# Kernel optimization log

Hardware: AMD Instinct MI355X
Metric: run time of the kernel (lower is better)

## Reference

```python
import jax, jax.numpy as jnp
import numpy as np
from jax import lax

KSIZE = 3      # match kernel
STRIDE = 1
RATE = 2       # dilation / downscale rate
FUSE_K = 3     # diagonal-fuse kernel
SCALE = 10.0   # softmax scale
FUSE = True
ESC = 1e-4     # escape_NaN, added per-element before the reduce_sum (as in torch code)


def _same_pad(x, k, s):
    # x: [C, H, W] -> zero-padded so that strided k-window 'same' extraction works
    C, H, W = x.shape
    oh, ow = -(-H // s), -(-W // s)
    ph = max(0, (oh - 1) * s + k - H)
    pw = max(0, (ow - 1) * s + k - W)
    xp = jnp.pad(x, ((0, 0), (ph // 2, ph - ph // 2), (pw // 2, pw - pw // 2)))
    return xp, oh, ow


def extract_patches(x, k, s):
    # x: [C, H, W] -> [L, C, k, k], L row-major over output grid (matches torch Unfold)
    C = x.shape[0]
    xp, oh, ow = _same_pad(x, k, s)
    cols = [xp[:, dh:dh + s * (oh - 1) + 1:s, dw:dw + s * (ow - 1) + 1:s]
            for dh in range(k) for dw in range(k)]
    p = jnp.stack(cols, 0).reshape(k, k, C, oh, ow)
    return p.transpose(3, 4, 2, 0, 1).reshape(oh * ow, C, k, k)


def fuse_diag(x):
    # conv with eye(FUSE_K) kernel, 'same' padding: sum of diagonal shifts
    A, B = x.shape
    pt = (FUSE_K - 1) // 2
    pb = FUSE_K - 1 - pt
    xp = jnp.pad(x, ((pt, pb), (pt, pb)))
    out = xp[0:A, 0:B]
    for d in range(1, FUSE_K):
        out = out + xp[d:d + A, d:d + B]
    return out


def _forward(f, b, mask):
    B, C, H, W = f.shape
    kernel = 2 * RATE
    # mask -> mm gate over background patches (shared across batch: torch uses m[0])
    mask_s = mask[0][:, ::4 * RATE, ::4 * RATE]           # [1, H/r, W/r] nearest downsample
    m = extract_patches(mask_s, KSIZE, STRIDE)            # [L, 1, k, k]
    mm = (jnp.mean(m, axis=(1, 2, 3)) == 0.0).astype(f.dtype)[:, None, None]  # [L,1,1]

    def single(fi, bi):
        # raw patches from full-res background for reconstruction: [Lb, C, 2r, 2r]
        raw_w = extract_patches(bi, kernel, RATE * STRIDE)
        # nearest 1/rate downsample
        fs = fi[:, ::RATE, ::RATE]
        bs = bi[:, ::RATE, ::RATE]
        bh, bw = bs.shape[1], bs.shape[2]
        fh, fw = fs.shape[1], fs.shape[2]
        Lb, Lf = bh * bw, fh * fw
        # match patches from downsampled background, L2-normalized per patch
        w = extract_patches(bs, KSIZE, STRIDE)                      # [Lb, C, 3, 3]
        denom = jnp.sqrt(jnp.sum(w * w + ESC, axis=(1, 2, 3), keepdims=True))
        wn = (w / denom).reshape(Lb, -1)                            # [Lb, C*9]
        # correlation = conv of fs with wn filters = patch GEMM
        fp = extract_patches(fs, KSIZE, 1).reshape(Lf, -1)          # [Lf, C*9]
        scores = wn @ fp.T                                          # [Lb, Lf]
        if FUSE:
            s = fuse_diag(scores)
            s = s.reshape(bh, bw, fh, fw).transpose(1, 0, 3, 2).reshape(Lb, Lf)
            s = fuse_diag(s)
            s = s.reshape(bw, bh, fw, fh).transpose(1, 0, 3, 2).reshape(Lb, Lf)
            scores = s
        att = scores.reshape(Lb, fh, fw) * mm
        att = jax.nn.softmax(att * SCALE, axis=0) * mm              # softmax over patches
        # conv_transpose2d(att, raw_w, stride=rate, padding=1) / 4
        rhs = jnp.flip(raw_w, (2, 3)).transpose(1, 0, 2, 3)         # [C, Lb, 2r, 2r] OIHW
        pad = kernel - 1 - 1                                        # k - 1 - torch_padding
        out = lax.conv_general_dilated(
            att[None], rhs, window_strides=(1, 1),
            padding=[(pad, pad), (pad, pad)], lhs_dilation=(RATE, RATE),
            dimension_numbers=('NCHW', 'OIHW', 'NCHW'))[0] / 4.0    # [C, H, W]
        return out

    return jax.vmap(single)(f, b)


def setup_inputs() -> dict:
    key = jax.random.key(0)
    k1, k2 = jax.random.split(key)
    B, C, H, W = 4, 128, 96, 96
    f = jax.random.normal(k1, (B, C, H, W), jnp.float32)
    b = jax.random.normal(k2, (B, C, H, W), jnp.float32)
    mask = jnp.zeros((1, 1, 4 * H, 4 * W), jnp.float32)
    mask = mask.at[:, :, 96:288, 96:288].set(1.0)
    return {"f": f, "b": b, "mask": mask}


def reference(f, b, mask):
    return _forward(f, b, mask)
```

## Files before the change

### kernel.cpp

```cpp
#include <hip/hip_runtime.h>

typedef _Float16 half8 __attribute__((ext_vector_type(8)));
typedef float floatx4 __attribute__((ext_vector_type(4)));

#define LBF 2304
#define K1  1152
#define LDK2 2304

__device__ __forceinline__ void gll16(const _Float16* g, _Float16* l) {
    __builtin_amdgcn_global_load_lds((const __attribute__((address_space(1))) void*)g,
                                     (__attribute__((address_space(3))) void*)l, 16, 0, 0);
}

__device__ __forceinline__ int dec_kc(int s) { return (s >= 0) ? s + 1 : -s - 1; }

__global__ void stage_scan(const float* __restrict__ f, const float* __restrict__ bsrc,
                           const float* __restrict__ mask,
                           float* __restrict__ ds, int* __restrict__ pos) {
    int tid = threadIdx.x;
    if (blockIdx.x < 9216) {
        long flat = (long)blockIdx.x * 256 + tid;
        int p = flat % 2304;
        long rest = flat / 2304;
        int c = rest % 128;
        int b = (rest / 128) % 4;
        int t = rest / (128 * 4);
        int pi = p / 48, pj = p % 48;
        const float* src = t ? bsrc : f;
        ds[flat] = src[(((long)b * 128 + c) * 96 + 2 * pi) * 96 + 2 * pj];
        return;
    }
    int mmb[9], loc[9]; int s = 0;
#pragma unroll
    for (int t = 0; t < 9; t++) {
        int p = tid * 9 + t;
        int pi = p / 48, pj = p % 48;
        float sm = 0.f;
#pragma unroll
        for (int u = 0; u < 3; u++)
#pragma unroll
            for (int v = 0; v < 3; v++) {
                int y = pi - 1 + u, x = pj - 1 + v;
                if ((unsigned)y < 48u && (unsigned)x < 48u)
                    sm += mask[(8 * y) * 384 + 8 * x];
            }
        int m = (sm == 0.f) ? 1 : 0;
        mmb[t] = m; loc[t] = s; s += m;
    }
    __shared__ int sh[256];
    sh[tid] = s; __syncthreads();
    for (int off = 1; off < 256; off <<= 1) {
        int v = (tid >= off) ? sh[tid - off] : 0;
        __syncthreads();
        sh[tid] += v;
        __syncthreads();
    }
    int excl = sh[tid] - s;
#pragma unroll
    for (int t = 0; t < 9; t++) {
        int e = excl + loc[t];
        pos[tid * 9 + t] = mmb[t] ? e : (-e - 1);
    }
}

__global__ void prep_fp(const float* __restrict__ ds, _Float16* __restrict__ fp) {
    int k = blockIdx.x * 128 + threadIdx.x;
    int p = blockIdx.y;
    int b = blockIdx.z;
    int c = k / 9, r = k % 9, u = r / 3, v = r % 3;
    int pi = p / 48, pj = p % 48;
    int y = pi - 1 + u, x = pj - 1 + v;
    float val = 0.f;
    if ((unsigned)y < 48u && (unsigned)x < 48u)
        val = ds[((long)(b * 128 + c)) * 2304 + y * 48 + x];
    fp[((long)b * LBF + p) * K1 + k] = (_Float16)val;
}

__global__ void prep_wn(const float* __restrict__ ds, _Float16* __restrict__ wn) {
    int p = blockIdx.x, b = blockIdx.y;
    int tid = threadIdx.x;
    int pi = p / 48, pj = p % 48;
    const float* dsb = ds + (long)(4 + b) * 128 * 2304;
    float w[9];
    float ss = 0.f;
#pragma unroll
    for (int t = 0; t < 9; t++) {
        int k = tid + t * 128;
        int c = k / 9, r = k % 9, u = r / 3, v = r % 3;
        int y = pi - 1 + u, x = pj - 1 + v;
        float val = 0.f;
        if ((unsigned)y < 48u && (unsigned)x < 48u)
            val = dsb[(long)c * 2304 + y * 48 + x];
        w[t] = val;
        ss += val * val;
    }
    for (int m = 32; m; m >>= 1) ss += __shfl_xor(ss, m);
    __shared__ float sh[2];
    if ((tid & 63) == 0) sh[tid >> 6] = ss;
    __syncthreads();
    float denom = sqrtf(sh[0] + sh[1] + 0.1152f);
    float inv = 1.f / denom;
#pragma unroll
    for (int t = 0; t < 9; t++) {
        int k = tid + t * 128;
        wn[((long)b * LBF + p) * K1 + k] = (_Float16)(w[t] * inv);
    }
}

__global__ void prep_wtc(const float* __restrict__ bsrc, const int* __restrict__ pos,
                         _Float16* __restrict__ wtc) {
    int p = blockIdx.x * 256 + threadIdx.x;
    int c = blockIdx.y;
    int b = blockIdx.z;
    int sp = pos[p];
    long base = ((long)b * 2048 + c * 16) * LDK2;
    if (sp < 0) {
        int kc = dec_kc(pos[2303]);
        int kp = (kc + 63) & ~63;
        int mo = p + sp + 1;
        if (mo < kp - kc) {
#pragma unroll
            for (int n = 0; n < 16; n++)
                wtc[base + (long)n * LDK2 + kc + mo] = (_Float16)0.f;
        }
        return;
    }
    int pi = p / 48, pj = p % 48;
    const float* src = bsrc + ((long)b * 128 + c) * 96 * 96;
#pragma unroll
    for (int u = 0; u < 4; u++) {
        int y = 2 * pi - 1 + u;
        bool yok = (unsigned)y < 96u;
#pragma unroll
        for (int v = 0; v < 4; v++) {
            int x = 2 * pj - 1 + v;
            float val = 0.f;
            if (yok && (unsigned)x < 96u) val = src[y * 96 + x];
            wtc[base + (long)(u * 4 + v) * LDK2 + sp] = (_Float16)val;
        }
    }
}

__device__ __forceinline__ void gemm_compute(const _Float16* lA, const _Float16* lB,
                                             floatx4 (&acc)[4][4],
                                             int wr, int wc, int lm, int pcp) {
    half8 af[4], bf[4];
#pragma unroll
    for (int t = 0; t < 4; t++) {
        af[t] = *(const half8*)&lA[(wr * 64 + t * 16 + lm) * 64 + pcp];
        bf[t] = *(const half8*)&lB[(wc * 64 + t * 16 + lm) * 64 + pcp];
    }
#pragma unroll
    for (int i = 0; i < 4; i++)
#pragma unroll
        for (int j = 0; j < 4; j++)
            acc[i][j] = __builtin_amdgcn_mfma_f32_16x16x32_f16(af[i], bf[j], acc[i][j], 0, 0, 0);
#pragma unroll
    for (int t = 0; t < 4; t++) {
        af[t] = *(const half8*)&lA[(wr * 64 + t * 16 + lm) * 64 + (pcp ^ 32)];
        bf[t] = *(const half8*)&lB[(wc * 64 + t * 16 + lm) * 64 + (pcp ^ 32)];
    }
#pragma unroll
    for (int i = 0; i < 4; i++)
#pragma unroll
        for (int j = 0; j < 4; j++)
            acc[i][j] = __builtin_amdgcn_mfma_f32_16x16x32_f16(af[i], bf[j], acc[i][j], 0, 0, 0);
}

__global__ __launch_bounds__(256)
void gemm_nt64(const _Float16* __restrict__ A, const _Float16* __restrict__ B,
               float* __restrict__ C, int M, int N, int ldk, int swapxy,
               const int* __restrict__ Kpos, int Kstat, long sA, long sB, long sC) {
    A += blockIdx.z * sA; B += blockIdx.z * sB; C += blockIdx.z * sC;
    int K;
    if (Kpos) { int kc = dec_kc(Kpos[0]); K = (kc + 63) & ~63; }
    else K = Kstat;
    const int tid = threadIdx.x;
    const int lane = tid & 63, wave = tid >> 6;
    const int wr = wave >> 1, wc = wave & 1;
    const int bm = swapxy ? blockIdx.x : blockIdx.y;
    const int bn = swapxy ? blockIdx.y : blockIdx.x;
    const int m0 = bm * 128, n0 = bn * 128;

    __shared__ _Float16 sm[4][128 * 64];

    floatx4 acc[4][4] = {};

    const int lm = lane & 15, q = lane >> 4;
    const int pcp = (q ^ (lm & 7)) * 8;

    const int srow8 = lane >> 3;
    const int gc = ((lane & 7) ^ srow8) * 8;
    const _Float16* gA[4]; const _Float16* gB[4];
    int dOff[4];
#pragma unroll
    for (int c = 0; c < 4; c++) {
        int r = (wave * 4 + c) * 8 + srow8;
        gA[c] = A + (long)(m0 + r) * ldk + gc;
        gB[c] = B + (long)(n0 + r) * ldk + gc;
        dOff[c] = (wave * 4 + c) * 512;
    }

    if (K > 0) {
#pragma unroll
        for (int c = 0; c < 4; c++) gll16(gA[c], &sm[0][dOff[c]]);
#pragma unroll
        for (int c = 0; c < 4; c++) gll16(gB[c], &sm[1][dOff[c]]);
        __syncthreads();
        int k0 = 0, buf = 0;
        while (true) {
            int kn = k0 + 64;
            if (kn < K) {
                const int nb = (buf ^ 1) * 2;
#pragma unroll
                for (int c = 0; c < 4; c++) gll16(gA[c] + kn, &sm[nb][dOff[c]]);
#pragma unroll
                for (int c = 0; c < 4; c++) gll16(gB[c] + kn, &sm[nb + 1][dOff[c]]);
            }
            gemm_compute(sm[buf * 2], sm[buf * 2 + 1], acc, wr, wc, lm, pcp);
            __syncthreads();
            k0 = kn; buf ^= 1;
            if (k0 >= K) break;
        }
    }

    const int col = n0 + wc * 64 + lm;
    const int rowq = q * 4;
#pragma unroll
    for (int i = 0; i < 4; i++) {
        int row = m0 + wr * 64 + i * 16 + rowq;
#pragma unroll
        for (int j = 0; j < 4; j++)
#pragma unroll
            for (int r = 0; r < 4; r++)
                C[(long)(row + r) * N + col + j * 16] = acc[i][j][r];
    }
}

__global__ __launch_bounds__(256)
void fuseA(const float* __restrict__ ST, float* __restrict__ FT1) {
    int y = blockIdx.x, bb = blockIdx.y;
    const float* S = ST + (long)bb * LBF * LBF;
    float* F = FT1 + (long)bb * LBF * LBF;
    const float* r0 = S + (long)(y > 0 ? y - 1 : 0) * LBF;
    const float* r1 = S + (long)y * LBF;
    const float* r2 = S + (long)(y < LBF - 1 ? y + 1 : y) * LBF;
    float m0 = (y > 0) ? 1.f : 0.f;
    float m2 = (y < LBF - 1) ? 1.f : 0.f;
    float* o = F + (long)y * LBF;
#pragma unroll
    for (int u = 0; u < 9; u++) {
        int x = threadIdx.x + u * 256;
        float lo = (x > 0) ? m0 * r0[x - 1] : 0.f;
        float hi = (x < LBF - 1) ? m2 * r2[x + 1] : 0.f;
        o[x] = lo + r1[x] + hi;
    }
}

__global__ __launch_bounds__(256)
void fuseB_softmax(const float* __restrict__ FT1, const int* __restrict__ pos,
                   _Float16* __restrict__ attTc_g) {
    int j = blockIdx.x, bb = blockIdx.y;
    int tid = threadIdx.x;
    const float* F = FT1 + (long)bb * LBF * LBF;
    _Float16* orow = attTc_g + ((long)bb * LBF + j) * LDK2;
    int Pj = (j % 48) * 48 + j / 48;
    long roff[3]; bool jok[3];
#pragma unroll
    for (int t = 0; t < 3; t++) {
        int j2 = Pj + t - 1;
        jok[t] = (unsigned)j2 < (unsigned)LBF;
        int jc = jok[t] ? j2 : 0;
        roff[t] = (long)((jc % 48) * 48 + jc / 48) * LBF;
    }
    float v[9]; int ps[9];
    float mx = -1e30f;
#pragma unroll
    for (int u = 0; u < 9; u++) {
        int x = tid + u * 256;
        int sp = pos[x];
        ps[u] = sp;
        float xv = 0.f;
        if (sp >= 0) {
            int a = x / 48, b = x - a * 48;
            int Px = b * 48 + a;
            float acc = 0.f;
#pragma unroll
            for (int t = 0; t < 3; t++) {
                int d2 = t - 1;
                int uu = Px + d2;
                if (jok[t] && (unsigned)uu < (unsigned)LBF) {
                    int ad = a + d2;
                    int c = ((unsigned)ad < 48u) ? (x + 48 * d2)
                          : (ad == 48 ? (b + 1) : (2255 + b));
                    acc += F[roff[t] + c];
                }
            }
            xv = acc * 10.f;
        }
        v[u] = xv;
        mx = fmaxf(mx, xv);
    }
    for (int m = 32; m; m >>= 1) mx = fmaxf(mx, __shfl_xor(mx, m));
    __shared__ float sh[4], sh2[4];
    if ((tid & 63) == 0) sh[tid >> 6] = mx;
    __syncthreads();
    mx = fmaxf(fmaxf(sh[0], sh[1]), fmaxf(sh[2], sh[3]));
    float sum = 0.f;
#pragma unroll
    for (int u = 0; u < 9; u++) { v[u] = __expf(v[u] - mx); sum += v[u]; }
    for (int m = 32; m; m >>= 1) sum += __shfl_xor(sum, m);
    if ((tid & 63) == 0) sh2[tid >> 6] = sum;
    __syncthreads();
    sum = sh2[0] + sh2[1] + sh2[2] + sh2[3];
    float inv = 1.f / sum;
#pragma unroll
    for (int u = 0; u < 9; u++) {
        if (ps[u] >= 0) orow[ps[u]] = (_Float16)(v[u] * inv);
    }
    int kc = dec_kc(pos[2303]);
    int kp = (kc + 63) & ~63;
    if (tid < kp - kc) orow[kc + tid] = (_Float16)0.f;
}

__global__ void scatter_out(const float* __restrict__ MT_, float* __restrict__ out) {
    int yx = blockIdx.x * 256 + threadIdx.x;
    int c = blockIdx.y, b = blockIdx.z;
    int y = yx / 96, x = yx % 96;
    const float* Mb = MT_ + (long)b * 2048 * LBF;
    float s = 0.f;
    for (int uu = (y + 1) & 1; uu < 4; uu += 2) {
        int fi = (y + 1 - uu) >> 1;
        if ((unsigned)fi >= 48u) continue;
        for (int vv = (x + 1) & 1; vv < 4; vv += 2) {
            int fj = (x + 1 - vv) >> 1;
            if ((unsigned)fj >= 48u) continue;
            s += Mb[(long)(c * 16 + uu * 4 + vv) * LBF + fi * 48 + fj];
        }
    }
    out[(((long)b * 128 + c) * 96 + y) * 96 + x] = 0.25f * s;
}

extern "C" void kernel_launch(void* const* d_in, const int* in_sizes, int n_in,
                              void* d_out, int out_size, void* d_ws, size_t ws_size,
                              hipStream_t stream) {
    const float* f    = (const float*)d_in[0];
    const float* bsrc = (const float*)d_in[1];
    const float* mask = (const float*)d_in[2];
    float* out = (float*)d_out;

    char* ws = (char*)d_ws;
    const size_t offR1  = 84934656;
    const size_t offWn  = offR1 + 21233664;
    const size_t offWtc = offR1 + 42467328;
    const size_t offFT1 = offWtc + 37748736;
    const size_t offPos = offFT1 + 2ul * 21233664;
    const size_t NEED   = offPos + 9216;
    if (ws_size < NEED) return;

    float*    ST    = (float*)(ws + 0);
    float*    MT    = (float*)(ws + 0);
    _Float16* fp    = (_Float16*)(ws + offR1);
    _Float16* wn    = (_Float16*)(ws + offWn);
    _Float16* attTc = (_Float16*)(ws + offR1);
    _Float16* Wtc   = (_Float16*)(ws + offWtc);
    float*    ds    = (float*)(ws + offFT1);
    float*    FT1   = (float*)(ws + offFT1);
    int*      pos   = (int*)(ws + offPos);

    stage_scan<<<dim3(9217), 256, 0, stream>>>(f, bsrc, mask, ds, pos);
    prep_fp<<<dim3(9, 2304, 4), 128, 0, stream>>>(ds, fp);
    prep_wn<<<dim3(2304, 4), 128, 0, stream>>>(ds, wn);
    prep_wtc<<<dim3(9, 128, 4), 256, 0, stream>>>(bsrc, pos, Wtc);

    gemm_nt64<<<dim3(18, 18, 4), 256, 0, stream>>>(fp, wn, ST, 2304, 2304, K1, 0,
        nullptr, K1, (long)2304 * K1, (long)2304 * K1, (long)2304 * 2304);

    for (int g = 0; g < 2; g++) {
        fuseA<<<dim3(LBF, 2), 256, 0, stream>>>(ST + (long)g * 2 * LBF * LBF, FT1);
        fuseB_softmax<<<dim3(LBF, 2), 256, 0, stream>>>(FT1, pos,
            attTc + (long)g * 2 * LBF * LDK2);
    }

    gemm_nt64<<<dim3(16, 18, 4), 256, 0, stream>>>(Wtc, attTc, MT, 2048, 2304, LDK2, 1,
        pos + 2303, 0, (long)2048 * LDK2, (long)2304 * LDK2, (long)2048 * 2304);

    scatter_out<<<dim3(36, 128, 4), 256, 0, stream>>>(MT, out);
}
```

Baseline: 470.0 us.

## Replace first GEMM with 256x128-tile, 4-stage LDS-pipelined kernel

```diff
diff --git a/kernel.cpp b/kernel.cpp
--- a/kernel.cpp
+++ b/kernel.cpp
@@ -141,6 +141,109 @@
     }
 }
 
+#define REGA 8192
+#define REGB 4096
+
+__global__ __launch_bounds__(512, 2)
+void gemm1_8ph(const _Float16* __restrict__ A, const _Float16* __restrict__ B,
+               float* __restrict__ C) {
+    extern __shared__ _Float16 smem[];
+    _Float16* SA = smem;
+    _Float16* SB = smem + 4 * REGA;
+
+    int bid = blockIdx.x;
+    int wg = (bid & 7) * 81 + (bid >> 3);
+    int z = wg / 162; int t = wg - z * 162;
+    const int m0 = (t / 18) * 256, n0 = (t % 18) * 128;
+
+    const _Float16* gA = A + (long)z * 2304 * K1 + (long)m0 * K1;
+    const _Float16* gB = B + (long)z * 2304 * K1 + (long)n0 * K1;
+    float* Cb = C + (long)z * 2304 * 2304;
+
+    const int tid = threadIdx.x;
+    const int wave = tid >> 6, lane = tid & 63;
+    const int lm = lane & 15, q = lane >> 4;
+    const int wm = wave >> 1, wn_ = wave & 1;
+    const int soff = (q ^ ((lm >> 1) & 3)) * 8;
+    const int srow = lane >> 2;
+    const int scol = (((lane & 3) ^ ((lane >> 3) & 3))) * 8;
+
+    floatx4 acc[4][4] = {};
+
+    auto stA = [&](int reg, int kcol) {
+        _Float16* dst = SA + reg * REGA;
+        gll16(gA + (long)(wave * 32 + srow) * K1 + kcol, dst + wave * 1024);
+        gll16(gA + (long)(wave * 32 + 16 + srow) * K1 + kcol, dst + wave * 1024 + 512);
+    };
+    auto stB = [&](int reg, int kcol) {
+        gll16(gB + (long)(wave * 16 + srow) * K1 + kcol, SB + reg * REGB + wave * 512);
+    };
+    auto ldA = [&](int reg, int i) -> half8 {
+        return *(const half8*)&SA[reg * REGA + (wm * 64 + i * 16 + lm) * 32 + soff];
+    };
+    auto ldB = [&](int reg, int j) -> half8 {
+        return *(const half8*)&SB[reg * REGB + (wn_ * 64 + j * 16 + lm) * 32 + soff];
+    };
+
+    stA(0, 0 + scol);  stB(0, 0 + scol);
+    stA(1, 32 + scol); stB(1, 32 + scol);
+    stA(2, 64 + scol); stB(2, 64 + scol);
+    asm volatile("s_waitcnt vmcnt(6)" ::: "memory");
+    __builtin_amdgcn_s_barrier();
+
+    for (int k = 0; k < 18; ++k) {
+        const int b = k & 1;
+        const int rg0 = b * 2, rg1 = rg0 + 1, og1 = (b ^ 1) * 2 + 1;
+        {
+            half8 af[4], bf[4];
+#pragma unroll
+            for (int i = 0; i < 4; ++i) af[i] = ldA(rg0, i);
+#pragma unroll
+            for (int j = 0; j < 4; ++j) bf[j] = ldB(rg0, j);
+            if (k + 1 < 18) { int kc = (k + 1) * 64 + 32 + scol; stA(og1, kc); stB(og1, kc); }
+            asm volatile("s_waitcnt vmcnt(6)" ::: "memory");
+            __builtin_amdgcn_s_barrier();
+            __builtin_amdgcn_s_setprio(1);
+#pragma unroll
+            for (int i = 0; i < 4; ++i)
+#pragma unroll
+                for (int j = 0; j < 4; ++j)
+                    acc[i][j] = __builtin_amdgcn_mfma_f32_16x16x32_f16(af[i], bf[j], acc[i][j], 0, 0, 0);
+            __builtin_amdgcn_s_setprio(0);
+            __builtin_amdgcn_s_barrier();
+        }
+        {
+            half8 af[4], bf[4];
+#pragma unroll
+            for (int i = 0; i < 4; ++i) af[i] = ldA(rg1, i);
+#pragma unroll
+            for (int j = 0; j < 4; ++j) bf[j] = ldB(rg1, j);
+            if (k + 2 < 18) { int kc = (k + 2) * 64 + scol; stA(rg0, kc); stB(rg0, kc); }
+            asm volatile("s_waitcnt vmcnt(6)" ::: "memory");
+            __builtin_amdgcn_s_barrier();
+            __builtin_amdgcn_s_setprio(1);
+#pragma unroll
+            for (int i = 0; i < 4; ++i)
+#pragma unroll
+                for (int j = 0; j < 4; ++j)
+                    acc[i][j] = __builtin_amdgcn_mfma_f32_16x16x32_f16(af[i], bf[j], acc[i][j], 0, 0, 0);
+            __builtin_amdgcn_s_setprio(0);
+            __builtin_amdgcn_s_barrier();
+        }
+    }
+
+    const int col = n0 + wn_ * 64 + lm;
+#pragma unroll
+    for (int i = 0; i < 4; ++i) {
+        const int row = m0 + wm * 64 + i * 16 + q * 4;
+#pragma unroll
+        for (int j = 0; j < 4; ++j)
+#pragma unroll
+            for (int r = 0; r < 4; ++r)
+                Cb[(long)(row + r) * 2304 + col + j * 16] = acc[i][j][r];
+    }
+}
+
 __device__ __forceinline__ void gemm_compute(const _Float16* lA, const _Float16* lB,
                                              floatx4 (&acc)[4][4],
                                              int wr, int wc, int lm, int pcp) {
@@ -373,8 +476,9 @@
     prep_wn<<<dim3(2304, 4), 128, 0, stream>>>(ds, wn);
     prep_wtc<<<dim3(9, 128, 4), 256, 0, stream>>>(bsrc, pos, Wtc);
 
-    gemm_nt64<<<dim3(18, 18, 4), 256, 0, stream>>>(fp, wn, ST, 2304, 2304, K1, 0,
-        nullptr, K1, (long)2304 * K1, (long)2304 * K1, (long)2304 * 2304);
+    hipFuncSetAttribute((const void*)gemm1_8ph,
+                        hipFuncAttributeMaxDynamicSharedMemorySize, 98304);
+    gemm1_8ph<<<dim3(648), 512, 98304, stream>>>(fp, wn, ST);
 
     for (int g = 0; g < 2; g++) {
         fuseA<<<dim3(LBF, 2), 256, 0, stream>>>(ST + (long)g * 2 * LBF * LBF, FT1);
```

Result: no change. 468.2 us (-0.4%).
